# Performance work log

Hardware: AMD Instinct MI355X
Metric: run time of the kernel (lower is better)

## Reference

```python
import jax, jax.numpy as jnp
import numpy as np

EPS = 1e-8
MARGIN = 0.1


def _l2_normalize(x):
    n = jnp.linalg.norm(x, axis=-1, keepdims=True)
    return x / jnp.clip(n, 1e-12)


def _euclidean_distance_matrix(x):
    dot = x @ x.T                      # (N, N)
    sq = jnp.diagonal(dot)             # (N,)
    d2 = jax.nn.relu(sq[None, :] - 2.0 * dot + sq[:, None])
    zmask = (d2 == 0.0).astype(x.dtype)
    d = jnp.sqrt(d2 + zmask * EPS)
    return d * (1.0 - zmask)


def _triplet_mask(labels):
    n = labels.shape[0]
    neq = ~jnp.eye(n, dtype=bool)
    distinct = neq[:, :, None] & neq[:, None, :] & neq[None, :, :]
    leq = labels[None, :] == labels[:, None]           # (N, N)
    valid = leq[:, :, None] & (~leq[:, None, :])       # i==j, i!=k
    return distinct & valid


def setup_inputs() -> dict:
    key = jax.random.key(0)
    k1, k2, k3 = jax.random.split(key, 3)
    B, D = 192, 512
    return {
        "output1": jax.random.normal(k1, (B, D), dtype=jnp.float32),
        "output2": jax.random.normal(k2, (B, D), dtype=jnp.float32),
        "weight": jax.random.uniform(k3, (B, B), dtype=jnp.float32),
    }


def reference(output1, output2, weight):
    B = output1.shape[0]
    o1 = _l2_normalize(output1)
    o2 = _l2_normalize(output2)
    emb = jnp.concatenate([o1, o2], axis=0)            # (2B, D)
    labels = jnp.concatenate([jnp.arange(B), jnp.arange(B)])

    dm = _euclidean_distance_matrix(emb)               # (2B, 2B)
    # triplet_loss[i, j, k] = d(i,j) - d(i,k) + margin
    tl = dm[:, :, None] - dm[:, None, :] + MARGIN      # (2B, 2B, 2B)
    mask = _triplet_mask(labels).astype(tl.dtype)
    tl = jax.nn.relu(tl * mask)

    # punished matrix: weight tiled 2x2 over (i, k), broadcast over j
    pm = jnp.tile(weight, (2, 2))                      # (2B, 2B)
    tl = tl * pm[:, None, :]
    num_pos = jnp.sum((tl > EPS).astype(tl.dtype))
    return jnp.sum(tl) / (num_pos + EPS)
```

## Files before the change

### kernel.cpp

```cpp
#include <hip/hip_runtime.h>

#define BB 192
#define NN 384
#define DD 512
#define EPSF 1e-8f
#define MARGINF 0.1f
#define BKT 128
#define PAD 34


__global__ void norms_kernel(const float* __restrict__ o1,
                             const float* __restrict__ o2,
                             float* __restrict__ ninv,
                             float* __restrict__ accum) {
    int w = threadIdx.x >> 6, lane = threadIdx.x & 63;
    int r = blockIdx.x * 4 + w;
    const float4* src = reinterpret_cast<const float4*>(
        (r < BB) ? o1 + (size_t)r * DD : o2 + (size_t)(r - BB) * DD);
    float4 v0 = src[lane], v1 = src[lane + 64];
    float ss = v0.x*v0.x + v0.y*v0.y + v0.z*v0.z + v0.w*v0.w
             + v1.x*v1.x + v1.y*v1.y + v1.z*v1.z + v1.w*v1.w;
    for (int off = 32; off >= 1; off >>= 1) ss += __shfl_xor(ss, off);
    if (lane == 0) ninv[r] = 1.0f / fmaxf(sqrtf(ss), 1e-12f);
    if (blockIdx.x == 0 && threadIdx.x == 0) { accum[0] = 0.0f; accum[1] = 0.0f; }
}

__global__ __launch_bounds__(256) void gram_kernel(const float* __restrict__ o1,
                                                   const float* __restrict__ o2,
                                                   float* __restrict__ Gout,
                                                   int klen) {
    __shared__ float As[BKT][PAD];
    __shared__ float Bs[BKT][PAD];
    int t = threadIdx.x;
    int bi = blockIdx.x, bk = blockIdx.y, bz = blockIdx.z;
    int ai0 = bi * 32, ki0 = bk * 32;
    const float4* Asrc = reinterpret_cast<const float4*>(
        (bi < 6) ? o1 + (size_t)ai0 * DD : o2 + (size_t)(ai0 - BB) * DD);
    const float4* Bsrc = reinterpret_cast<const float4*>(
        (bk < 6) ? o1 + (size_t)ki0 * DD : o2 + (size_t)(ki0 - BB) * DD);
    int tx = t & 15, ty = t >> 4;
    float acc00 = 0.f, acc01 = 0.f, acc10 = 0.f, acc11 = 0.f;
    int kbase4 = bz * (klen >> 2);
    int nkt = klen / BKT;
    for (int kt = 0; kt < nkt; ++kt) {
        int k04 = kbase4 + kt * (BKT / 4);
        __syncthreads();
        #pragma unroll
        for (int j = 0; j < 4; ++j) {
            int id = j * 256 + t;
            int row = id >> 5, c4 = id & 31;
            float4 va = Asrc[(size_t)row * (DD / 4) + k04 + c4];
            float4 vb = Bsrc[(size_t)row * (DD / 4) + k04 + c4];
            int kk = c4 << 2;
            As[kk][row] = va.x; As[kk + 1][row] = va.y;
            As[kk + 2][row] = va.z; As[kk + 3][row] = va.w;
            Bs[kk][row] = vb.x; Bs[kk + 1][row] = vb.y;
            Bs[kk + 2][row] = vb.z; Bs[kk + 3][row] = vb.w;
        }
        __syncthreads();
        #pragma unroll 8
        for (int kk = 0; kk < BKT; ++kk) {
            float2 a = *reinterpret_cast<const float2*>(&As[kk][ty * 2]);
            float2 b = *reinterpret_cast<const float2*>(&Bs[kk][tx * 2]);
            acc00 += a.x * b.x; acc01 += a.x * b.y;
            acc10 += a.y * b.x; acc11 += a.y * b.y;
        }
    }
    float* g = Gout + (size_t)bz * NN * NN;
    int gi = ai0 + ty * 2, gk = ki0 + tx * 2;
    g[(size_t)gi * NN + gk]       = acc00;
    g[(size_t)gi * NN + gk + 1]   = acc01;
    g[(size_t)(gi + 1) * NN + gk]     = acc10;
    g[(size_t)(gi + 1) * NN + gk + 1] = acc11;
}

__global__ void loss_kernel(const float* __restrict__ G,
                            const float* __restrict__ ninv,
                            const float* __restrict__ weight,
                            float* __restrict__ accum,
                            int nslab) {
    int i = blockIdx.x;
    int t = threadIdx.x;
    int w = t >> 6, lane = t & 63;
    int ib = (i < BB) ? i : i - BB;
    int p  = (i < BB) ? i + BB : i - BB;
    float ninv_i = ninv[i];
    const float* Gi  = G + (size_t)i * NN;
    const float* Gi2 = Gi + (size_t)NN * NN;

    float gp = Gi[p] + ((nslab == 2) ? Gi2[p] : 0.0f);
    float cosp = gp * ninv_i * ninv[p];
    float d2p = fmaxf(0.0f, 2.0f - 2.0f * cosp);
    float dpos = (d2p > 0.0f) ? sqrtf(d2p) : 0.0f;

    float lsum = 0.0f, lcnt = 0.0f;
    for (int k = t; k < NN; k += 256) {
        int kb = (k < BB) ? k : k - BB;
        if (kb == ib) continue;
        float g = Gi[k] + ((nslab == 2) ? Gi2[k] : 0.0f);
        float c = g * ninv_i * ninv[k];
        float d2 = fmaxf(0.0f, 2.0f - 2.0f * c);
        float dik = (d2 > 0.0f) ? sqrtf(d2) : 0.0f;
        float tl = dpos - dik + MARGINF;
        if (tl > 0.0f) {
            float v = tl * weight[(size_t)ib * BB + kb];
            lsum += v;
            if (v > EPSF) lcnt += 1.0f;
        }
    }
    for (int off = 32; off >= 1; off >>= 1) {
        lsum += __shfl_xor(lsum, off);
        lcnt += __shfl_xor(lcnt, off);
    }
    __shared__ float ssum[4], scnt[4];
    if (lane == 0) { ssum[w] = lsum; scnt[w] = lcnt; }
    __syncthreads();
    if (t == 0) {
        atomicAdd(&accum[0], ssum[0] + ssum[1] + ssum[2] + ssum[3]);
        atomicAdd(&accum[1], scnt[0] + scnt[1] + scnt[2] + scnt[3]);
    }
}

__global__ void finalize_kernel(const float* __restrict__ accum,
                                float* __restrict__ out) {
    if (threadIdx.x == 0 && blockIdx.x == 0)
        out[0] = accum[0] / (accum[1] + EPSF);
}

extern "C" void kernel_launch(void* const* d_in, const int* in_sizes, int n_in,
                              void* d_out, int out_size, void* d_ws, size_t ws_size,
                              hipStream_t stream) {
    const float* o1 = (const float*)d_in[0];
    const float* o2 = (const float*)d_in[1];
    const float* w  = (const float*)d_in[2];
    float* out = (float*)d_out;

    float* ws_f  = (float*)d_ws;
    float* ninv  = ws_f;
    float* accum = ws_f + NN;
    float* G     = ws_f + 512;

    size_t need2 = (size_t)(512 + 2 * NN * NN) * sizeof(float);
    int KS = (ws_size >= need2) ? 2 : 1;

    norms_kernel<<<NN / 4, 256, 0, stream>>>(o1, o2, ninv, accum);
    gram_kernel<<<dim3(12, 12, KS), 256, 0, stream>>>(o1, o2, G, DD / KS);
    loss_kernel<<<NN, 256, 0, stream>>>(G, ninv, w, accum, KS);
    finalize_kernel<<<1, 64, 0, stream>>>(accum, out);
}
```

Before: 84.05 us.

## Fuse norm computation into Gram diagonal and finalize into loss via ticket

The separate norms kernel is dropped; inverse norms are taken from the diagonal of the raw Gram matrix inside the gram kernel. The finalize kernel is replaced by a last-block ticket counter in the loss kernel, and the K-split over two slabs is removed so each Gram block covers the full depth. This cuts the launch count from four to two, at the cost of a 144-block gram grid with a longer serial K loop.

```diff
diff --git a/kernel.cpp b/kernel.cpp
--- a/kernel.cpp
+++ b/kernel.cpp
@@ -9,30 +9,19 @@
 #define PAD 34
 
 
-__global__ void norms_kernel(const float* __restrict__ o1,
-                             const float* __restrict__ o2,
-                             float* __restrict__ ninv,
-                             float* __restrict__ accum) {
-    int w = threadIdx.x >> 6, lane = threadIdx.x & 63;
-    int r = blockIdx.x * 4 + w;
-    const float4* src = reinterpret_cast<const float4*>(
-        (r < BB) ? o1 + (size_t)r * DD : o2 + (size_t)(r - BB) * DD);
-    float4 v0 = src[lane], v1 = src[lane + 64];
-    float ss = v0.x*v0.x + v0.y*v0.y + v0.z*v0.z + v0.w*v0.w
-             + v1.x*v1.x + v1.y*v1.y + v1.z*v1.z + v1.w*v1.w;
-    for (int off = 32; off >= 1; off >>= 1) ss += __shfl_xor(ss, off);
-    if (lane == 0) ninv[r] = 1.0f / fmaxf(sqrtf(ss), 1e-12f);
-    if (blockIdx.x == 0 && threadIdx.x == 0) { accum[0] = 0.0f; accum[1] = 0.0f; }
-}
-
 __global__ __launch_bounds__(256) void gram_kernel(const float* __restrict__ o1,
                                                    const float* __restrict__ o2,
-                                                   float* __restrict__ Gout,
-                                                   int klen) {
+                                                   float* __restrict__ G,
+                                                   float* __restrict__ ninv,
+                                                   float* __restrict__ accum,
+                                                   unsigned* __restrict__ ticket) {
+    int t = threadIdx.x;
+    int bi = blockIdx.x, bk = blockIdx.y;
+    if (bi == 0 && bk == 0 && t == 0) {
+        accum[0] = 0.0f; accum[1] = 0.0f; *ticket = 0u;
+    }
     __shared__ float As[BKT][PAD];
     __shared__ float Bs[BKT][PAD];
-    int t = threadIdx.x;
-    int bi = blockIdx.x, bk = blockIdx.y, bz = blockIdx.z;
     int ai0 = bi * 32, ki0 = bk * 32;
     const float4* Asrc = reinterpret_cast<const float4*>(
         (bi < 6) ? o1 + (size_t)ai0 * DD : o2 + (size_t)(ai0 - BB) * DD);
@@ -40,10 +29,8 @@
         (bk < 6) ? o1 + (size_t)ki0 * DD : o2 + (size_t)(ki0 - BB) * DD);
     int tx = t & 15, ty = t >> 4;
     float acc00 = 0.f, acc01 = 0.f, acc10 = 0.f, acc11 = 0.f;
-    int kbase4 = bz * (klen >> 2);
-    int nkt = klen / BKT;
-    for (int kt = 0; kt < nkt; ++kt) {
-        int k04 = kbase4 + kt * (BKT / 4);
+    for (int kt = 0; kt < DD / BKT; ++kt) {
+        int k04 = kt * (BKT / 4);
         __syncthreads();
         #pragma unroll
         for (int j = 0; j < 4; ++j) {
@@ -66,30 +53,32 @@
             acc10 += a.y * b.x; acc11 += a.y * b.y;
         }
     }
-    float* g = Gout + (size_t)bz * NN * NN;
     int gi = ai0 + ty * 2, gk = ki0 + tx * 2;
-    g[(size_t)gi * NN + gk]       = acc00;
-    g[(size_t)gi * NN + gk + 1]   = acc01;
-    g[(size_t)(gi + 1) * NN + gk]     = acc10;
-    g[(size_t)(gi + 1) * NN + gk + 1] = acc11;
+    G[(size_t)gi * NN + gk]           = acc00;
+    G[(size_t)gi * NN + gk + 1]       = acc01;
+    G[(size_t)(gi + 1) * NN + gk]     = acc10;
+    G[(size_t)(gi + 1) * NN + gk + 1] = acc11;
+    if (bi == bk && tx == ty) {
+        ninv[gi]     = 1.0f / fmaxf(sqrtf(acc00), 1e-12f);
+        ninv[gi + 1] = 1.0f / fmaxf(sqrtf(acc11), 1e-12f);
+    }
 }
 
 __global__ void loss_kernel(const float* __restrict__ G,
                             const float* __restrict__ ninv,
                             const float* __restrict__ weight,
                             float* __restrict__ accum,
-                            int nslab) {
+                            unsigned* __restrict__ ticket,
+                            float* __restrict__ out) {
     int i = blockIdx.x;
     int t = threadIdx.x;
     int w = t >> 6, lane = t & 63;
     int ib = (i < BB) ? i : i - BB;
     int p  = (i < BB) ? i + BB : i - BB;
     float ninv_i = ninv[i];
-    const float* Gi  = G + (size_t)i * NN;
-    const float* Gi2 = Gi + (size_t)NN * NN;
+    const float* Gi = G + (size_t)i * NN;
 
-    float gp = Gi[p] + ((nslab == 2) ? Gi2[p] : 0.0f);
-    float cosp = gp * ninv_i * ninv[p];
+    float cosp = Gi[p] * ninv_i * ninv[p];
     float d2p = fmaxf(0.0f, 2.0f - 2.0f * cosp);
     float dpos = (d2p > 0.0f) ? sqrtf(d2p) : 0.0f;
 
@@ -97,8 +86,7 @@
     for (int k = t; k < NN; k += 256) {
         int kb = (k < BB) ? k : k - BB;
         if (kb == ib) continue;
-        float g = Gi[k] + ((nslab == 2) ? Gi2[k] : 0.0f);
-        float c = g * ninv_i * ninv[k];
+        float c = Gi[k] * ninv_i * ninv[k];
         float d2 = fmaxf(0.0f, 2.0f - 2.0f * c);
         float dik = (d2 > 0.0f) ? sqrtf(d2) : 0.0f;
         float tl = dpos - dik + MARGINF;
@@ -118,13 +106,14 @@
     if (t == 0) {
         atomicAdd(&accum[0], ssum[0] + ssum[1] + ssum[2] + ssum[3]);
         atomicAdd(&accum[1], scnt[0] + scnt[1] + scnt[2] + scnt[3]);
+        __threadfence();
+        unsigned r = atomicAdd(ticket, 1u);
+        if (r == NN - 1) {
+            float s = atomicAdd(&accum[0], 0.0f);
+            float c = atomicAdd(&accum[1], 0.0f);
+            out[0] = s / (c + EPSF);
+        }
     }
-}
-
-__global__ void finalize_kernel(const float* __restrict__ accum,
-                                float* __restrict__ out) {
-    if (threadIdx.x == 0 && blockIdx.x == 0)
-        out[0] = accum[0] / (accum[1] + EPSF);
 }
 
 extern "C" void kernel_launch(void* const* d_in, const int* in_sizes, int n_in,
@@ -135,16 +124,12 @@
     const float* w  = (const float*)d_in[2];
     float* out = (float*)d_out;
 
-    float* ws_f  = (float*)d_ws;
-    float* ninv  = ws_f;
-    float* accum = ws_f + NN;
-    float* G     = ws_f + 512;
+    float* ws_f      = (float*)d_ws;
+    float* ninv      = ws_f;
+    float* accum     = ws_f + NN;
+    unsigned* ticket = (unsigned*)(ws_f + NN + 2);
+    float* G         = ws_f + 512;
 
-    size_t need2 = (size_t)(512 + 2 * NN * NN) * sizeof(float);
-    int KS = (ws_size >= need2) ? 2 : 1;
-
-    norms_kernel<<<NN / 4, 256, 0, stream>>>(o1, o2, ninv, accum);
-    gram_kernel<<<dim3(12, 12, KS), 256, 0, stream>>>(o1, o2, G, DD / KS);
-    loss_kernel<<<NN, 256, 0, stream>>>(G, ninv, w, accum, KS);
-    finalize_kernel<<<1, 64, 0, stream>>>(accum, out);
+    gram_kernel<<<dim3(12, 12), 256, 0, stream>>>(o1, o2, G, ninv, accum, ticket);
+    loss_kernel<<<NN, 256, 0, stream>>>(G, ninv, w, accum, ticket, out);
 }
```

After: 86.84 us. +3.3%, slower.
